# Performance work log

Measured on AMD Instinct MI355X. Metric: run time of the kernel, lower is better.

Reference implementation:

```python
import jax, jax.numpy as jnp
import numpy as np

N = 100000      # nodes
E = 3200000     # edges (avg degree 32)
DIN, DH, DOUT = 128, 32, 2


def setup_inputs() -> dict:
    key = jax.random.key(0)
    k1, k2, k3, k4 = jax.random.split(key, 4)
    x = jax.random.normal(k1, (N, DIN), dtype=jnp.float32)
    edge_index = jax.random.randint(k2, (2, E), 0, N, dtype=jnp.int64)
    # Glorot-ish scaled weights
    W1 = jax.random.normal(k3, (DIN, DH), dtype=jnp.float32) / np.sqrt(DIN)
    b1 = jnp.zeros((DH,), dtype=jnp.float32)
    W2 = jax.random.normal(k4, (DH, DOUT), dtype=jnp.float32) / np.sqrt(DH)
    b2 = jnp.zeros((DOUT,), dtype=jnp.float32)
    return {"x": x, "edge_index": edge_index, "W1": W1, "b1": b1, "W2": W2, "b2": b2}


def reference(x, edge_index, W1, b1, W2, b2):
    n = x.shape[0]
    # GCNConv default: add self-loops, symmetric deg^{-1/2} A deg^{-1/2} normalization
    loops = jnp.arange(n, dtype=edge_index.dtype)
    src = jnp.concatenate([edge_index[0], loops])  # [E+N]
    dst = jnp.concatenate([edge_index[1], loops])  # [E+N]
    deg = jax.ops.segment_sum(jnp.ones_like(dst, dtype=x.dtype), dst, num_segments=n)
    dinv = jnp.where(deg > 0, jax.lax.rsqrt(deg), 0.0)
    norm = dinv[src] * dinv[dst]  # [E+N]

    def gcn_layer(h, W, b):
        m = h @ W                                   # [n, dout] transform first (PyG order)
        msgs = m[src] * norm[:, None]               # gather + scale  [E+N, dout]
        agg = jax.ops.segment_sum(msgs, dst, num_segments=n)  # scatter-add
        return agg + b

    h = jax.nn.relu(gcn_layer(x, W1, b1))
    return gcn_layer(h, W2, b2)
```

## Files before the change

kernel.cpp:

```cpp
#include <hip/hip_runtime.h>
#include <hip/hip_bf16.h>

#define DIN 128
#define DH 32
#define DOUT 2
#define NPB 128
#define NPB_SHIFT 7
#define NBUK_MAX 1024
#define FILL_EDGES 8192
#define ECHUNK 2048

#define FXS1 262144.0f
#define FXI1 (1.0f / 262144.0f)
#define FXS2 131072.0f
#define FXI2 (1.0f / 131072.0f)


__device__ inline unsigned short f2bf(float f) {
    unsigned int u = __float_as_uint(f);
    u = (u + 0x7FFFu + ((u >> 16) & 1u)) >> 16;
    return (unsigned short)u;
}
__device__ inline float bfLO(unsigned int w) { return __uint_as_float(w << 16); }
__device__ inline float bfHI(unsigned int w) { return __uint_as_float(w & 0xFFFF0000u); }

__global__ void zero_gcnt_kernel(int* __restrict__ gcnt, int nbuk) {
    int i = blockIdx.x * blockDim.x + threadIdx.x;
    if (i < nbuk) gcnt[i] = 0;
}

__global__ void bukhist_kernel(const int* __restrict__ dst, int* __restrict__ gcnt,
                               int e, int nbuk) {
    __shared__ int lcnt[NBUK_MAX];
    int t = threadIdx.x;
    for (int i = t; i < nbuk; i += 256) lcnt[i] = 0;
    __syncthreads();
    int e0 = blockIdx.x * FILL_EDGES;
    int m = min(FILL_EDGES, e - e0);
    for (int i = t; i < m; i += 256) atomicAdd(&lcnt[dst[e0 + i] >> NPB_SHIFT], 1);
    __syncthreads();
    for (int i = t; i < nbuk; i += 256)
        if (lcnt[i]) atomicAdd(&gcnt[i], lcnt[i]);
}

__global__ void scan_kernel(const int* __restrict__ gcnt, int* __restrict__ gbase,
                            int* __restrict__ gcur, int nbuk,
                            unsigned short* __restrict__ mqc, int n) {
    __shared__ int sd[256];
    int t = threadIdx.x;
    if (t < 16) ((unsigned int*)(mqc + (size_t)n * DH))[t] = 0u;
    int v[4], s = 0;
#pragma unroll
    for (int k = 0; k < 4; ++k) {
        int i = 4 * t + k;
        v[k] = (i < nbuk) ? gcnt[i] : 0;
        s += v[k];
    }
    sd[t] = s;
    __syncthreads();
    for (int off = 1; off < 256; off <<= 1) {
        int x = (t >= off) ? sd[t - off] : 0;
        __syncthreads();
        sd[t] += x;
        __syncthreads();
    }
    int run = sd[t] - s;
#pragma unroll
    for (int k = 0; k < 4; ++k) {
        int i = 4 * t + k;
        if (i < nbuk) { gbase[i] = run; gcur[i] = run; }
        run += v[k];
    }
}

__global__ void binfill_kernel(const int* __restrict__ src, const int* __restrict__ dst,
                               int* __restrict__ gcur, unsigned int* __restrict__ binned,
                               int e, int nbuk) {
    __shared__ int cnt[NBUK_MAX];
    __shared__ int pos[NBUK_MAX];
    __shared__ int gb[NBUK_MAX];
    __shared__ unsigned int sorted[FILL_EDGES];
    __shared__ unsigned short aux[FILL_EDGES];
    __shared__ int stmp[256];

    int t = threadIdx.x;
    int e0 = blockIdx.x * FILL_EDGES;
    int m = min(FILL_EDGES, e - e0);

    for (int i = t; i < nbuk; i += 256) cnt[i] = 0;
    __syncthreads();
    for (int i = t; i < m; i += 256) atomicAdd(&cnt[dst[e0 + i] >> NPB_SHIFT], 1);
    __syncthreads();

    int v[4], s = 0;
#pragma unroll
    for (int k = 0; k < 4; ++k) {
        int i = 4 * t + k;
        v[k] = (i < nbuk) ? cnt[i] : 0;
        s += v[k];
    }
    stmp[t] = s;
    __syncthreads();
    for (int off = 1; off < 256; off <<= 1) {
        int x = (t >= off) ? stmp[t - off] : 0;
        __syncthreads();
        stmp[t] += x;
        __syncthreads();
    }
    int run = stmp[t] - s;
#pragma unroll
    for (int k = 0; k < 4; ++k) {
        int i = 4 * t + k;
        if (i < nbuk) pos[i] = run;
        run += v[k];
    }
    __syncthreads();

    for (int i = t; i < m; i += 256) {
        int d = dst[e0 + i];
        int sv = src[e0 + i];
        int b = d >> NPB_SHIFT;
        int r = atomicAdd(&pos[b], 1);
        sorted[r] = ((unsigned int)(d & (NPB - 1)) << 17) | (unsigned int)sv;
        aux[r] = (unsigned short)b;
    }
    __syncthreads();

    for (int b = t; b < nbuk; b += 256) {
        int c = cnt[b];
        gb[b] = c ? atomicAdd(&gcur[b], c) : 0;
    }
    __syncthreads();

    for (int i = t; i < m; i += 256) {
        int b = aux[i];
        int start = pos[b] - cnt[b];
        binned[gb[b] + (i - start)] = sorted[i];
    }
}

__global__ void bdinv_kernel(const int* __restrict__ gbase, const int* __restrict__ gcnt,
                             const unsigned int* __restrict__ binned,
                             float* __restrict__ dinv, int n) {
    __shared__ int cnt[NPB];
    int t = threadIdx.x;
    int b = blockIdx.x;
    if (t < NPB) cnt[t] = 0;
    __syncthreads();
    const int beg = gbase[b];
    const int cntb = gcnt[b];
    for (int i = t; i < cntb; i += 256) atomicAdd(&cnt[binned[beg + i] >> 17], 1);
    __syncthreads();
    if (t < NPB) {
        int r = (b << NPB_SHIFT) + t;
        if (r < n) dinv[r] = rsqrtf((float)(cnt[t] + 1));
    }
}

#define XLD 132
__global__ void gemm1_kernel(const float* __restrict__ x, const float* __restrict__ W1,
                             const float* __restrict__ dinv,
                             unsigned short* __restrict__ mqc, int n) {
    __shared__ float  Xl[32 * XLD];
    __shared__ float4 Wl4[DIN * 8];

    int t = threadIdx.x;
    for (int i = t; i < DIN * 8; i += 256) Wl4[i] = ((const float4*)W1)[i];

    int rb = blockIdx.x * 32;
    for (int i = t; i < 32 * 32; i += 256) {
        int rr = i >> 5, c4 = i & 31;
        int gr = rb + rr;
        float4 v = make_float4(0.f, 0.f, 0.f, 0.f);
        if (gr < n) v = ((const float4*)x)[(size_t)gr * 32 + c4];
        ((float4*)Xl)[rr * 33 + c4] = v;
    }
    __syncthreads();

    const int lane = t & 7;
    const int row  = t >> 3;
    const float* xrow = &Xl[row * XLD];
    float4 acc = make_float4(0.f, 0.f, 0.f, 0.f);
#pragma unroll
    for (int k = 0; k < DIN; ++k) {
        float xv = xrow[k];
        float4 w = Wl4[k * 8 + lane];
        acc.x += xv * w.x; acc.y += xv * w.y;
        acc.z += xv * w.z; acc.w += xv * w.w;
    }
    int r = rb + row;
    if (r < n) {
        float di = dinv[r];
        ushort4 sv;
        sv.x = f2bf(acc.x * di); sv.y = f2bf(acc.y * di);
        sv.z = f2bf(acc.z * di); sv.w = f2bf(acc.w * di);
        *(ushort4*)&mqc[(size_t)r * DH + 4 * lane] = sv;
    }
}

__global__ void __launch_bounds__(512, 8)
agg1_kernel(const int* __restrict__ gbase, const int* __restrict__ gcnt,
            const unsigned int* __restrict__ binned,
            const unsigned short* __restrict__ mqc,
            const float* __restrict__ dinv,
            const float* __restrict__ b1, const float* __restrict__ W2,
            float2* __restrict__ m2q, int n) {
    __shared__ int acc[NPB * 33];
    __shared__ unsigned int ebuf[2][ECHUNK];

    const int t = threadIdx.x;
    const int b = blockIdx.x;
    const int beg = gbase[b];
    const int cntb = gcnt[b];
    const int r0 = b << NPB_SHIFT;

    for (int i = t; i < NPB * 33; i += 512) acc[i] = 0;

    const unsigned int* __restrict__ bp = binned + beg;
    const unsigned int* __restrict__ mq32 = (const unsigned int*)mqc;
    const unsigned int sent = (unsigned int)n;
    const int nchunks = (cntb + ECHUNK - 1) / ECHUNK;

    unsigned int st[4];
    if (nchunks > 0) {
#pragma unroll
        for (int k = 0; k < 4; ++k) {
            int idx = t + k * 512;
            st[k] = (idx < cntb) ? __builtin_nontemporal_load(&bp[idx]) : sent;
        }
#pragma unroll
        for (int k = 0; k < 4; ++k) ebuf[0][t + k * 512] = st[k];
    }
    __syncthreads();

    const int g = t >> 4, l = t & 15;

    for (int c = 0; c < nchunks; ++c) {
        if (c + 1 < nchunks) {
            const int base = (c + 1) * ECHUNK;
#pragma unroll
            for (int k = 0; k < 4; ++k) {
                int idx = base + t + k * 512;
                st[k] = (idx < cntb) ? __builtin_nontemporal_load(&bp[idx]) : sent;
            }
        }
        const unsigned int* eb = ebuf[c & 1];
        for (int j = 0; j < 64; j += 8) {
            const unsigned int* ej = &eb[g + 32 * j];
            unsigned int e0 = ej[0],   e1 = ej[32],  e2 = ej[64],  e3 = ej[96];
            unsigned int e4 = ej[128], e5 = ej[160], e6 = ej[192], e7 = ej[224];
            unsigned int w0 = mq32[(e0 & 0x1FFFFu) * 16u + l];
            unsigned int w1 = mq32[(e1 & 0x1FFFFu) * 16u + l];
            unsigned int w2 = mq32[(e2 & 0x1FFFFu) * 16u + l];
            unsigned int w3 = mq32[(e3 & 0x1FFFFu) * 16u + l];
            unsigned int w4 = mq32[(e4 & 0x1FFFFu) * 16u + l];
            unsigned int w5 = mq32[(e5 & 0x1FFFFu) * 16u + l];
            unsigned int w6 = mq32[(e6 & 0x1FFFFu) * 16u + l];
            unsigned int w7 = mq32[(e7 & 0x1FFFFu) * 16u + l];
            int d0 = (int)(e0 >> 17) * 33 + 2 * l;
            int d1 = (int)(e1 >> 17) * 33 + 2 * l;
            int d2 = (int)(e2 >> 17) * 33 + 2 * l;
            int d3 = (int)(e3 >> 17) * 33 + 2 * l;
            int d4 = (int)(e4 >> 17) * 33 + 2 * l;
            int d5 = (int)(e5 >> 17) * 33 + 2 * l;
            int d6 = (int)(e6 >> 17) * 33 + 2 * l;
            int d7 = (int)(e7 >> 17) * 33 + 2 * l;
            atomicAdd(&acc[d0], __float2int_rn(bfLO(w0) * FXS1));
            atomicAdd(&acc[d0 + 1], __float2int_rn(bfHI(w0) * FXS1));
            atomicAdd(&acc[d1], __float2int_rn(bfLO(w1) * FXS1));
            atomicAdd(&acc[d1 + 1], __float2int_rn(bfHI(w1) * FXS1));
            atomicAdd(&acc[d2], __float2int_rn(bfLO(w2) * FXS1));
            atomicAdd(&acc[d2 + 1], __float2int_rn(bfHI(w2) * FXS1));
            atomicAdd(&acc[d3], __float2int_rn(bfLO(w3) * FXS1));
            atomicAdd(&acc[d3 + 1], __float2int_rn(bfHI(w3) * FXS1));
            atomicAdd(&acc[d4], __float2int_rn(bfLO(w4) * FXS1));
            atomicAdd(&acc[d4 + 1], __float2int_rn(bfHI(w4) * FXS1));
            atomicAdd(&acc[d5], __float2int_rn(bfLO(w5) * FXS1));
            atomicAdd(&acc[d5 + 1], __float2int_rn(bfHI(w5) * FXS1));
            atomicAdd(&acc[d6], __float2int_rn(bfLO(w6) * FXS1));
            atomicAdd(&acc[d6 + 1], __float2int_rn(bfHI(w6) * FXS1));
            atomicAdd(&acc[d7], __float2int_rn(bfLO(w7) * FXS1));
            atomicAdd(&acc[d7 + 1], __float2int_rn(bfHI(w7) * FXS1));
        }
        __syncthreads();
        if (c + 1 < nchunks) {
#pragma unroll
            for (int k = 0; k < 4; ++k) ebuf[(c + 1) & 1][t + k * 512] = st[k];
        }
        __syncthreads();
    }

    const int j = t >> 2, q = t & 3;
    const int r = r0 + j;
    if (r < n) {
        const float di = dinv[r];
        const unsigned int* srow = mq32 + (size_t)r * 16 + q * 4;
        const int* ar = &acc[j * 33 + q * 8];
        float p0 = 0.f, p1 = 0.f;
#pragma unroll
        for (int k = 0; k < 4; ++k) {
            unsigned int sw = srow[k];
            int c = q * 8 + 2 * k;
            float a0 = (float)ar[2 * k]     * FXI1;
            float a1 = (float)ar[2 * k + 1] * FXI1;
            float h0 = fmaxf(di * (a0 + bfLO(sw)) + b1[c],     0.0f);
            float h1 = fmaxf(di * (a1 + bfHI(sw)) + b1[c + 1], 0.0f);
            p0 += h0 * W2[2 * c]     + h1 * W2[2 * c + 2];
            p1 += h0 * W2[2 * c + 1] + h1 * W2[2 * c + 3];
        }
        p0 += __shfl_down(p0, 2, 4); p0 += __shfl_down(p0, 1, 4);
        p1 += __shfl_down(p1, 2, 4); p1 += __shfl_down(p1, 1, 4);
        if (q == 0) m2q[r] = make_float2(di * p0, di * p1);
    }
}

__global__ void __launch_bounds__(256, 4)
agg2_kernel(const int* __restrict__ gbase, const int* __restrict__ gcnt,
            const unsigned int* __restrict__ binned,
            const float2* __restrict__ m2q,
            const float* __restrict__ dinv, const float* __restrict__ b2,
            float* __restrict__ out, int n) {
    __shared__ int a0s[NPB], a1s[NPB];
    const int t = threadIdx.x;
    const int b = blockIdx.x;
    const int beg = gbase[b];
    const int cntb = gcnt[b];
    const int r0 = b << NPB_SHIFT;

    if (t < NPB) { a0s[t] = 0; a1s[t] = 0; }
    __syncthreads();

    const unsigned int* __restrict__ bp = binned + beg;
    int i = t;
    for (; i + 768 < cntb; i += 1024) {
        unsigned int e0 = __builtin_nontemporal_load(&bp[i]);
        unsigned int e1 = __builtin_nontemporal_load(&bp[i + 256]);
        unsigned int e2 = __builtin_nontemporal_load(&bp[i + 512]);
        unsigned int e3 = __builtin_nontemporal_load(&bp[i + 768]);
        float2 v0 = m2q[e0 & 0x1FFFFu];
        float2 v1 = m2q[e1 & 0x1FFFFu];
        float2 v2 = m2q[e2 & 0x1FFFFu];
        float2 v3 = m2q[e3 & 0x1FFFFu];
        atomicAdd(&a0s[e0 >> 17], __float2int_rn(v0.x * FXS2));
        atomicAdd(&a1s[e0 >> 17], __float2int_rn(v0.y * FXS2));
        atomicAdd(&a0s[e1 >> 17], __float2int_rn(v1.x * FXS2));
        atomicAdd(&a1s[e1 >> 17], __float2int_rn(v1.y * FXS2));
        atomicAdd(&a0s[e2 >> 17], __float2int_rn(v2.x * FXS2));
        atomicAdd(&a1s[e2 >> 17], __float2int_rn(v2.y * FXS2));
        atomicAdd(&a0s[e3 >> 17], __float2int_rn(v3.x * FXS2));
        atomicAdd(&a1s[e3 >> 17], __float2int_rn(v3.y * FXS2));
    }
    for (; i < cntb; i += 256) {
        unsigned int e0 = __builtin_nontemporal_load(&bp[i]);
        float2 v0 = m2q[e0 & 0x1FFFFu];
        atomicAdd(&a0s[e0 >> 17], __float2int_rn(v0.x * FXS2));
        atomicAdd(&a1s[e0 >> 17], __float2int_rn(v0.y * FXS2));
    }
    __syncthreads();

    if (t < NPB) {
        int r = r0 + t;
        if (r < n) {
            float di = dinv[r];
            float2 self = m2q[r];
            out[(size_t)r * DOUT + 0] = di * ((float)a0s[t] * FXI2 + self.x) + b2[0];
            out[(size_t)r * DOUT + 1] = di * ((float)a1s[t] * FXI2 + self.y) + b2[1];
        }
    }
}

extern "C" void kernel_launch(void* const* d_in, const int* in_sizes, int n_in,
                              void* d_out, int out_size, void* d_ws, size_t ws_size,
                              hipStream_t stream) {
    const float* x  = (const float*)d_in[0];
    const int*   ei = (const int*)d_in[1];
    const float* W1 = (const float*)d_in[2];
    const float* b1 = (const float*)d_in[3];
    const float* W2 = (const float*)d_in[4];
    const float* b2 = (const float*)d_in[5];
    float* out = (float*)d_out;

    const int n = in_sizes[0] / DIN;
    const int e = in_sizes[1] / 2;
    const int* src = ei;
    const int* dst = ei + e;
    const int nbuk = (n + NPB - 1) >> NPB_SHIFT;

    char* ws = (char*)d_ws;
    float* dinv   = (float*)ws;          ws += (size_t)n * 4;
    int* gcnt     = (int*)ws;            ws += NBUK_MAX * 4;
    int* gbase    = (int*)ws;            ws += NBUK_MAX * 4;
    int* gcur     = (int*)ws;            ws += NBUK_MAX * 4;
    unsigned int* binned = (unsigned int*)ws;   ws += (size_t)e * 4;
    unsigned short* mqc  = (unsigned short*)ws; ws += ((size_t)n + 1) * DH * 2;
    float2* m2q   = (float2*)ws;

    const int B = 256;
    const int fill_blocks = (e + FILL_EDGES - 1) / FILL_EDGES;

    zero_gcnt_kernel<<<(nbuk + B - 1) / B, B, 0, stream>>>(gcnt, nbuk);
    bukhist_kernel<<<fill_blocks, B, 0, stream>>>(dst, gcnt, e, nbuk);
    scan_kernel<<<1, B, 0, stream>>>(gcnt, gbase, gcur, nbuk, mqc, n);
    binfill_kernel<<<fill_blocks, B, 0, stream>>>(src, dst, gcur, binned, e, nbuk);
    bdinv_kernel<<<nbuk, B, 0, stream>>>(gbase, gcnt, binned, dinv, n);
    gemm1_kernel<<<(n + 31) / 32, B, 0, stream>>>(x, W1, dinv, mqc, n);
    agg1_kernel<<<nbuk, 512, 0, stream>>>(gbase, gcnt, binned, mqc, dinv, b1, W2, m2q, n);
    agg2_kernel<<<nbuk, B, 0, stream>>>(gbase, gcnt, binned, m2q, dinv, b2, out, n);
}
```

Measured before the change: 242.7 us.

## Store layer-1 messages as int16 fixed-point and register-block gemm1

The layer-1 transformed features are now quantized in gemm1 to 16-bit fixed point with scale 2048, replacing bf16. Aggregation can then add the sign-extended integers straight into the LDS atomics without float conversion. agg1 now fetches 8 bytes per lane (4 features) with 8 lanes per edge and software-prefetches the next group of gathers. gemm1 is rewritten with a transposed X tile and 4x4 register blocking per thread. The coarser fixed-point scale reduces precision and risks int16 overflow or saturation for large scaled values.

```diff
diff --git a/kernel.cpp b/kernel.cpp
--- a/kernel.cpp
+++ b/kernel.cpp
@@ -10,19 +10,16 @@
 #define FILL_EDGES 8192
 #define ECHUNK 2048
 
-#define FXS1 262144.0f
-#define FXI1 (1.0f / 262144.0f)
+#define FXS1 2048.0f
+#define FXI1 (1.0f / 2048.0f)
 #define FXS2 131072.0f
 #define FXI2 (1.0f / 131072.0f)
 
 
-__device__ inline unsigned short f2bf(float f) {
-    unsigned int u = __float_as_uint(f);
-    u = (u + 0x7FFFu + ((u >> 16) & 1u)) >> 16;
-    return (unsigned short)u;
-}
 __device__ inline float bfLO(unsigned int w) { return __uint_as_float(w << 16); }
 __device__ inline float bfHI(unsigned int w) { return __uint_as_float(w & 0xFFFF0000u); }
+__device__ inline int sxlo(unsigned int w) { return (int)(short)(w & 0xFFFFu); }
+__device__ inline int sxhi(unsigned int w) { return ((int)w) >> 16; }
 
 __global__ void zero_gcnt_kernel(int* __restrict__ gcnt, int nbuk) {
     int i = blockIdx.x * blockDim.x + threadIdx.x;
@@ -45,7 +42,7 @@
 
 __global__ void scan_kernel(const int* __restrict__ gcnt, int* __restrict__ gbase,
                             int* __restrict__ gcur, int nbuk,
-                            unsigned short* __restrict__ mqc, int n) {
+                            short* __restrict__ mqc, int n) {
     __shared__ int sd[256];
     int t = threadIdx.x;
     if (t < 16) ((unsigned int*)(mqc + (size_t)n * DH))[t] = 0u;
@@ -157,51 +154,63 @@
     }
 }
 
-#define XLD 132
-__global__ void gemm1_kernel(const float* __restrict__ x, const float* __restrict__ W1,
-                             const float* __restrict__ dinv,
-                             unsigned short* __restrict__ mqc, int n) {
-    __shared__ float  Xl[32 * XLD];
+#define XTS 68
+__global__ void __launch_bounds__(128, 4)
+gemm1_kernel(const float* __restrict__ x, const float* __restrict__ W1,
+             const float* __restrict__ dinv,
+             short* __restrict__ mqc, int n) {
+    __shared__ float  XT[DIN * XTS];
     __shared__ float4 Wl4[DIN * 8];
 
     int t = threadIdx.x;
-    for (int i = t; i < DIN * 8; i += 256) Wl4[i] = ((const float4*)W1)[i];
-
-    int rb = blockIdx.x * 32;
-    for (int i = t; i < 32 * 32; i += 256) {
-        int rr = i >> 5, c4 = i & 31;
-        int gr = rb + rr;
+    for (int i = t; i < DIN * 8; i += 128) Wl4[i] = ((const float4*)W1)[i];
+
+    int rb = blockIdx.x * 64;
+    for (int i = t; i < 64 * 32; i += 128) {
+        int r = i & 63, kq = i >> 6;
+        int gr = rb + r;
         float4 v = make_float4(0.f, 0.f, 0.f, 0.f);
-        if (gr < n) v = ((const float4*)x)[(size_t)gr * 32 + c4];
-        ((float4*)Xl)[rr * 33 + c4] = v;
-    }
-    __syncthreads();
-
-    const int lane = t & 7;
-    const int row  = t >> 3;
-    const float* xrow = &Xl[row * XLD];
-    float4 acc = make_float4(0.f, 0.f, 0.f, 0.f);
-#pragma unroll
+        if (gr < n) v = ((const float4*)x)[(size_t)gr * 32 + kq];
+        XT[(4 * kq + 0) * XTS + r] = v.x;
+        XT[(4 * kq + 1) * XTS + r] = v.y;
+        XT[(4 * kq + 2) * XTS + r] = v.z;
+        XT[(4 * kq + 3) * XTS + r] = v.w;
+    }
+    __syncthreads();
+
+    const int cq = t & 7;
+    const int rq = t >> 3;
+    float4 a0 = make_float4(0.f, 0.f, 0.f, 0.f);
+    float4 a1 = a0, a2 = a0, a3 = a0;
+#pragma unroll 4
     for (int k = 0; k < DIN; ++k) {
-        float xv = xrow[k];
-        float4 w = Wl4[k * 8 + lane];
-        acc.x += xv * w.x; acc.y += xv * w.y;
-        acc.z += xv * w.z; acc.w += xv * w.w;
-    }
-    int r = rb + row;
-    if (r < n) {
-        float di = dinv[r];
-        ushort4 sv;
-        sv.x = f2bf(acc.x * di); sv.y = f2bf(acc.y * di);
-        sv.z = f2bf(acc.z * di); sv.w = f2bf(acc.w * di);
-        *(ushort4*)&mqc[(size_t)r * DH + 4 * lane] = sv;
+        float4 xv = *(const float4*)&XT[k * XTS + 4 * rq];
+        float4 w  = Wl4[k * 8 + cq];
+        a0.x += xv.x * w.x; a0.y += xv.x * w.y; a0.z += xv.x * w.z; a0.w += xv.x * w.w;
+        a1.x += xv.y * w.x; a1.y += xv.y * w.y; a1.z += xv.y * w.z; a1.w += xv.y * w.w;
+        a2.x += xv.z * w.x; a2.y += xv.z * w.y; a2.z += xv.z * w.z; a2.w += xv.z * w.w;
+        a3.x += xv.w * w.x; a3.y += xv.w * w.y; a3.z += xv.w * w.z; a3.w += xv.w * w.w;
+    }
+#pragma unroll
+    for (int m = 0; m < 4; ++m) {
+        int r = rb + 4 * rq + m;
+        if (r < n) {
+            float di = dinv[r] * FXS1;
+            float4 av = (m == 0) ? a0 : (m == 1) ? a1 : (m == 2) ? a2 : a3;
+            short4 sv;
+            sv.x = (short)__float2int_rn(av.x * di);
+            sv.y = (short)__float2int_rn(av.y * di);
+            sv.z = (short)__float2int_rn(av.z * di);
+            sv.w = (short)__float2int_rn(av.w * di);
+            *(short4*)&mqc[(size_t)r * DH + 4 * cq] = sv;
+        }
     }
 }
 
 __global__ void __launch_bounds__(512, 8)
 agg1_kernel(const int* __restrict__ gbase, const int* __restrict__ gcnt,
             const unsigned int* __restrict__ binned,
-            const unsigned short* __restrict__ mqc,
+            const short* __restrict__ mqc,
             const float* __restrict__ dinv,
             const float* __restrict__ b1, const float* __restrict__ W2,
             float2* __restrict__ m2q, int n) {
@@ -217,7 +226,7 @@
     for (int i = t; i < NPB * 33; i += 512) acc[i] = 0;
 
     const unsigned int* __restrict__ bp = binned + beg;
-    const unsigned int* __restrict__ mq32 = (const unsigned int*)mqc;
+    const uint2* __restrict__ mqr = (const uint2*)mqc;
     const unsigned int sent = (unsigned int)n;
     const int nchunks = (cntb + ECHUNK - 1) / ECHUNK;
 
@@ -233,7 +242,9 @@
     }
     __syncthreads();
 
-    const int g = t >> 4, l = t & 15;
+    const int g = t >> 3;
+    const int l = t & 7;
+    const int lbase = 4 * l;
 
     for (int c = 0; c < nchunks; ++c) {
         if (c + 1 < nchunks) {
@@ -245,42 +256,34 @@
             }
         }
         const unsigned int* eb = ebuf[c & 1];
-        for (int j = 0; j < 64; j += 8) {
-            const unsigned int* ej = &eb[g + 32 * j];
-            unsigned int e0 = ej[0],   e1 = ej[32],  e2 = ej[64],  e3 = ej[96];
-            unsigned int e4 = ej[128], e5 = ej[160], e6 = ej[192], e7 = ej[224];
-            unsigned int w0 = mq32[(e0 & 0x1FFFFu) * 16u + l];
-            unsigned int w1 = mq32[(e1 & 0x1FFFFu) * 16u + l];
-            unsigned int w2 = mq32[(e2 & 0x1FFFFu) * 16u + l];
-            unsigned int w3 = mq32[(e3 & 0x1FFFFu) * 16u + l];
-            unsigned int w4 = mq32[(e4 & 0x1FFFFu) * 16u + l];
-            unsigned int w5 = mq32[(e5 & 0x1FFFFu) * 16u + l];
-            unsigned int w6 = mq32[(e6 & 0x1FFFFu) * 16u + l];
-            unsigned int w7 = mq32[(e7 & 0x1FFFFu) * 16u + l];
-            int d0 = (int)(e0 >> 17) * 33 + 2 * l;
-            int d1 = (int)(e1 >> 17) * 33 + 2 * l;
-            int d2 = (int)(e2 >> 17) * 33 + 2 * l;
-            int d3 = (int)(e3 >> 17) * 33 + 2 * l;
-            int d4 = (int)(e4 >> 17) * 33 + 2 * l;
-            int d5 = (int)(e5 >> 17) * 33 + 2 * l;
-            int d6 = (int)(e6 >> 17) * 33 + 2 * l;
-            int d7 = (int)(e7 >> 17) * 33 + 2 * l;
-            atomicAdd(&acc[d0], __float2int_rn(bfLO(w0) * FXS1));
-            atomicAdd(&acc[d0 + 1], __float2int_rn(bfHI(w0) * FXS1));
-            atomicAdd(&acc[d1], __float2int_rn(bfLO(w1) * FXS1));
-            atomicAdd(&acc[d1 + 1], __float2int_rn(bfHI(w1) * FXS1));
-            atomicAdd(&acc[d2], __float2int_rn(bfLO(w2) * FXS1));
-            atomicAdd(&acc[d2 + 1], __float2int_rn(bfHI(w2) * FXS1));
-            atomicAdd(&acc[d3], __float2int_rn(bfLO(w3) * FXS1));
-            atomicAdd(&acc[d3 + 1], __float2int_rn(bfHI(w3) * FXS1));
-            atomicAdd(&acc[d4], __float2int_rn(bfLO(w4) * FXS1));
-            atomicAdd(&acc[d4 + 1], __float2int_rn(bfHI(w4) * FXS1));
-            atomicAdd(&acc[d5], __float2int_rn(bfLO(w5) * FXS1));
-            atomicAdd(&acc[d5 + 1], __float2int_rn(bfHI(w5) * FXS1));
-            atomicAdd(&acc[d6], __float2int_rn(bfLO(w6) * FXS1));
-            atomicAdd(&acc[d6 + 1], __float2int_rn(bfHI(w6) * FXS1));
-            atomicAdd(&acc[d7], __float2int_rn(bfLO(w7) * FXS1));
-            atomicAdd(&acc[d7 + 1], __float2int_rn(bfHI(w7) * FXS1));
+
+        unsigned int ew[2][4];
+        uint2 wv[2][4];
+#pragma unroll
+        for (int u = 0; u < 4; ++u) ew[0][u] = eb[g + 64 * u];
+#pragma unroll
+        for (int u = 0; u < 4; ++u)
+            wv[0][u] = mqr[(size_t)(ew[0][u] & 0x1FFFFu) * 8u + l];
+
+#pragma unroll
+        for (int s = 0; s < 8; ++s) {
+            const int cur = s & 1, nxt = cur ^ 1;
+            if (s < 7) {
+#pragma unroll
+                for (int u = 0; u < 4; ++u) ew[nxt][u] = eb[g + 64 * (4 * (s + 1) + u)];
+#pragma unroll
+                for (int u = 0; u < 4; ++u)
+                    wv[nxt][u] = mqr[(size_t)(ew[nxt][u] & 0x1FFFFu) * 8u + l];
+            }
+#pragma unroll
+            for (int u = 0; u < 4; ++u) {
+                int* ap = &acc[(int)(ew[cur][u] >> 17) * 33 + lbase];
+                unsigned int wx = wv[cur][u].x, wy = wv[cur][u].y;
+                atomicAdd(&ap[0], sxlo(wx));
+                atomicAdd(&ap[1], sxhi(wx));
+                atomicAdd(&ap[2], sxlo(wy));
+                atomicAdd(&ap[3], sxhi(wy));
+            }
         }
         __syncthreads();
         if (c + 1 < nchunks) {
@@ -294,17 +297,15 @@
     const int r = r0 + j;
     if (r < n) {
         const float di = dinv[r];
-        const unsigned int* srow = mq32 + (size_t)r * 16 + q * 4;
+        const unsigned int* srow = (const unsigned int*)mqc + (size_t)r * 16 + q * 4;
         const int* ar = &acc[j * 33 + q * 8];
         float p0 = 0.f, p1 = 0.f;
 #pragma unroll
         for (int k = 0; k < 4; ++k) {
             unsigned int sw = srow[k];
             int c = q * 8 + 2 * k;
-            float a0 = (float)ar[2 * k]     * FXI1;
-            float a1 = (float)ar[2 * k + 1] * FXI1;
-            float h0 = fmaxf(di * (a0 + bfLO(sw)) + b1[c],     0.0f);
-            float h1 = fmaxf(di * (a1 + bfHI(sw)) + b1[c + 1], 0.0f);
+            float h0 = fmaxf(di * (float)(ar[2 * k]     + sxlo(sw)) * FXI1 + b1[c],     0.0f);
+            float h1 = fmaxf(di * (float)(ar[2 * k + 1] + sxhi(sw)) * FXI1 + b1[c + 1], 0.0f);
             p0 += h0 * W2[2 * c]     + h1 * W2[2 * c + 2];
             p1 += h0 * W2[2 * c + 1] + h1 * W2[2 * c + 3];
         }
@@ -392,7 +393,7 @@
     int* gbase    = (int*)ws;            ws += NBUK_MAX * 4;
     int* gcur     = (int*)ws;            ws += NBUK_MAX * 4;
     unsigned int* binned = (unsigned int*)ws;   ws += (size_t)e * 4;
-    unsigned short* mqc  = (unsigned short*)ws; ws += ((size_t)n + 1) * DH * 2;
+    short* mqc    = (short*)ws;          ws += ((size_t)n + 1) * DH * 2;
     float2* m2q   = (float2*)ws;
 
     const int B = 256;
@@ -403,7 +404,7 @@
     scan_kernel<<<1, B, 0, stream>>>(gcnt, gbase, gcur, nbuk, mqc, n);
     binfill_kernel<<<fill_blocks, B, 0, stream>>>(src, dst, gcur, binned, e, nbuk);
     bdinv_kernel<<<nbuk, B, 0, stream>>>(gbase, gcnt, binned, dinv, n);
-    gemm1_kernel<<<(n + 31) / 32, B, 0, stream>>>(x, W1, dinv, mqc, n);
+    gemm1_kernel<<<(n + 63) / 64, 128, 0, stream>>>(x, W1, dinv, mqc, n);
     agg1_kernel<<<nbuk, 512, 0, stream>>>(gbase, gcnt, binned, mqc, dinv, b1, W2, m2q, n);
     agg2_kernel<<<nbuk, B, 0, stream>>>(gbase, gcnt, binned, m2q, dinv, b2, out, n);
 }
```

Measured after the change: 256.9 us. +5.9%, slower.
